# Kernel optimization log

Hardware: AMD Instinct MI355X
Metric: run time of the kernel (lower is better)

The kernel has to match this reference:

```python
import jax, jax.numpy as jnp
import numpy as np

USER_NUM = 100000
ITEM_NUM = 50000
N_NODES = USER_NUM + ITEM_NUM
EMB = 64
LAYERS = 3
NNZ = 2400000


def spmm(rows, cols, vals, x, n):
    # sparse [n, n] (COO) @ dense [n, d] -> [n, d]
    gathered = vals[:, None] * x[cols]          # [nnz, d]
    return jax.ops.segment_sum(gathered, rows, num_segments=n)


def setup_inputs() -> dict:
    key = jax.random.key(0)
    ks = jax.random.split(key, 7)
    return {
        "user_emb": jax.random.normal(ks[0], (USER_NUM, EMB), jnp.float32) * 0.1,
        "item_emb": jax.random.normal(ks[1], (ITEM_NUM, EMB), jnp.float32) * 0.1,
        "w1": jax.random.normal(ks[2], (LAYERS, EMB, EMB), jnp.float32) * (1.0 / np.sqrt(EMB)),
        "w2": jax.random.normal(ks[3], (LAYERS, EMB, EMB), jnp.float32) * (1.0 / np.sqrt(EMB)),
        "adj_vals": jax.random.uniform(ks[4], (NNZ,), jnp.float32) * (1.0 / 16.0),
        "adj_rows": jax.random.randint(ks[5], (NNZ,), 0, N_NODES, jnp.int32),
        "adj_cols": jax.random.randint(ks[6], (NNZ,), 0, N_NODES, jnp.int32),
    }


def reference(user_emb, item_emb, w1, w2, adj_vals, adj_rows, adj_cols):
    ego = jnp.concatenate([user_emb, item_emb], axis=0)   # [N, d]
    n = ego.shape[0]
    all_emb = [ego]
    for k in range(w1.shape[0]):
        temp = ego @ w1[k]                                # [N, d]
        agg_temp = spmm(adj_rows, adj_cols, adj_vals, temp, n)
        agg_ego = spmm(adj_rows, adj_cols, adj_vals, ego, n)
        ego = jax.nn.leaky_relu(agg_temp + temp + (agg_ego * ego) @ w2[k])
        all_emb.append(ego)
    mean_emb = jnp.mean(jnp.stack(all_emb, axis=1), axis=1)  # [N, d]
    u = user_emb.shape[0]
    return mean_emb[:u], mean_emb[u:]
```

## Files before the change

kernel.cpp:

```cpp
#include <hip/hip_runtime.h>
#include <hip/hip_fp16.h>

typedef _Float16 f16;
typedef _Float16 f16x4 __attribute__((ext_vector_type(4)));
typedef _Float16 f16x8 __attribute__((ext_vector_type(8)));
typedef float f32x4 __attribute__((ext_vector_type(4)));

__device__ __forceinline__ float h2f(__half v) { return __half2float(v); }
__device__ __forceinline__ __half f2h(float v) { return __float2half(v); }

#define SCAN_CHUNK 2048
#define ASTRIDE 136

#define BSHIFT 8
#define BROWS (1 << BSHIFT)
#define MAXB 1024
#define TILE 4096
#define BCAP 5120

#define WT_ELEMS (64 * ASTRIDE)
#define WT_DWORDS (WT_ELEMS / 2)

__global__ void zero_out_kernel(float* __restrict__ out, int total) {
    int i = blockIdx.x * blockDim.x + threadIdx.x;
    if (i < total) out[i] = 0.0f;
}

__global__ void setup_kernel(const float* __restrict__ user, const float* __restrict__ item,
                             __half* __restrict__ ego0, int usz, int ND,
                             const float* __restrict__ w1, const float* __restrict__ w2,
                             f16* __restrict__ wt_pre, int L,
                             int* __restrict__ gcur, int nbuck) {
    int i = blockIdx.x * blockDim.x + threadIdx.x;
    if (i < ND) {
        float f = (i < usz) ? user[i] : item[i - usz];
        ego0[i] = f2h(f);
    }
    if (i < L * WT_ELEMS) {
        int layer = i / WT_ELEMS;
        int r = i % WT_ELEMS;
        int c = r / ASTRIDE, k = r % ASTRIDE;
        float v = 0.f;
        if (k < 64)       v = w1[(size_t)layer * 4096 + (size_t)k * 64 + c];
        else if (k < 128) v = w2[(size_t)layer * 4096 + (size_t)(k - 64) * 64 + c];
        wt_pre[i] = (f16)v;
    }
    if (i < nbuck) gcur[i] = i * BCAP;
}

__global__ void hist_kernel(const int* __restrict__ rows, int* __restrict__ cnt, int nnz) {
    int i = blockIdx.x * blockDim.x + threadIdx.x;
    if (i < nnz) atomicAdd(&cnt[rows[i]], 1);
}

__global__ void scan_pass1(const int* __restrict__ cnt, int* __restrict__ bsum, int n) {
    __shared__ int wt[4];
    int tid = threadIdx.x;
    int base = blockIdx.x * SCAN_CHUNK + tid * 8;
    int s = 0;
    #pragma unroll
    for (int k = 0; k < 8; ++k) { int i = base + k; if (i < n) s += cnt[i]; }
    #pragma unroll
    for (int o = 32; o > 0; o >>= 1) s += __shfl_down(s, o, 64);
    int lane = tid & 63, wid = tid >> 6;
    if (lane == 0) wt[wid] = s;
    __syncthreads();
    if (tid == 0) bsum[blockIdx.x] = wt[0] + wt[1] + wt[2] + wt[3];
}

__global__ void scan_pass2(int* __restrict__ bsum, int nb, int* __restrict__ total) {
    if (threadIdx.x == 0) {
        int run = 0;
        for (int b = 0; b < nb; ++b) { int v = bsum[b]; bsum[b] = run; run += v; }
        *total = run;
    }
}

__global__ void scan_pass3(int* __restrict__ cnt, const int* __restrict__ bsum,
                           int* __restrict__ rptr, int n, const int* __restrict__ total) {
    __shared__ int wt[4];
    int tid = threadIdx.x;
    int base = blockIdx.x * SCAN_CHUNK + tid * 8;
    int v[8];
    int s = 0;
    #pragma unroll
    for (int k = 0; k < 8; ++k) { int i = base + k; v[k] = (i < n) ? cnt[i] : 0; s += v[k]; }
    int lane = tid & 63, wid = tid >> 6;
    int xs = s;
    #pragma unroll
    for (int o = 1; o < 64; o <<= 1) { int t = __shfl_up(xs, o, 64); if (lane >= o) xs += t; }
    if (lane == 63) wt[wid] = xs;
    __syncthreads();
    int wexcl = 0;
    for (int w = 0; w < wid; ++w) wexcl += wt[w];
    int run = bsum[blockIdx.x] + wexcl + (xs - s);
    #pragma unroll
    for (int k = 0; k < 8; ++k) {
        int i = base + k;
        if (i < n) { rptr[i] = run; cnt[i] = run; }
        run += v[k];
    }
    if (blockIdx.x == 0 && tid == 0) rptr[n] = *total;
}

__global__ void scatter_kernel(const int* __restrict__ rows, const int* __restrict__ cols,
                               const float* __restrict__ vals, int* __restrict__ cursor,
                               int2* __restrict__ edges, int nnz) {
    int i = blockIdx.x * blockDim.x + threadIdx.x;
    if (i >= nnz) return;
    int r = rows[i];
    int pos = atomicAdd(&cursor[r], 1);
    edges[pos] = make_int2(cols[i], __float_as_int(vals[i]));
}

__global__ __launch_bounds__(256)
void binA_kernel(const int* __restrict__ rows, const int* __restrict__ cols,
                 const float* __restrict__ vals, int* __restrict__ gcur,
                 int2* __restrict__ bucketed, int nnz, int nbuck) {
    __shared__ int hist[MAXB];
    __shared__ int offs[MAXB];
    __shared__ int rbase[MAXB];
    __shared__ int2 reorder[TILE];
    __shared__ unsigned short slotb[TILE];
    __shared__ int wsum[4];
    int tid = threadIdx.x;
    int tbase = blockIdx.x * TILE;
    int cnt_here = min(TILE, nnz - tbase);

    for (int b = tid; b < MAXB; b += 256) hist[b] = 0;
    __syncthreads();

    int myrow[16]; int mycol[16]; float myval[16];
    #pragma unroll
    for (int k = 0; k < 16; ++k) {
        int i = tbase + tid + k * 256;
        int r = (i < nnz) ? rows[i] : -1;
        myrow[k] = r;
        if (r >= 0) {
            mycol[k] = cols[i];
            myval[k] = vals[i];
            atomicAdd(&hist[r >> BSHIFT], 1);
        }
    }
    __syncthreads();

    int b0 = tid * 4;
    int s0 = hist[b0], s1 = hist[b0 + 1], s2 = hist[b0 + 2], s3 = hist[b0 + 3];
    int tsum = s0 + s1 + s2 + s3;
    int lane = tid & 63, wid = tid >> 6;
    int x = tsum;
    #pragma unroll
    for (int o = 1; o < 64; o <<= 1) { int t = __shfl_up(x, o, 64); if (lane >= o) x += t; }
    if (lane == 63) wsum[wid] = x;
    __syncthreads();
    int wexcl = 0;
    for (int w = 0; w < wid; ++w) wexcl += wsum[w];
    int excl = wexcl + x - tsum;
    offs[b0]     = excl;
    offs[b0 + 1] = excl + s0;
    offs[b0 + 2] = excl + s0 + s1;
    offs[b0 + 3] = excl + s0 + s1 + s2;
    for (int b = tid; b < nbuck; b += 256) {
        int c = hist[b];
        rbase[b] = (c > 0) ? atomicAdd(&gcur[b], c) : 0;
    }
    __syncthreads();
    for (int b = tid; b < MAXB; b += 256) hist[b] = 0;
    __syncthreads();

    #pragma unroll
    for (int k = 0; k < 16; ++k) {
        int r = myrow[k];
        if (r >= 0) {
            int b = r >> BSHIFT;
            int p = offs[b] + atomicAdd(&hist[b], 1);
            reorder[p] = make_int2(((r & (BROWS - 1)) << 20) | mycol[k], __float_as_int(myval[k]));
            slotb[p] = (unsigned short)b;
        }
    }
    __syncthreads();

    for (int t = tid; t < cnt_here; t += 256) {
        int b = slotb[t];
        int dst = rbase[b] + (t - offs[b]);
        if (dst < (b + 1) * BCAP) bucketed[dst] = reorder[t];
    }
}

__global__ __launch_bounds__(256)
void binB_kernel(const int* __restrict__ gcur, const int2* __restrict__ bucketed,
                 int2* __restrict__ edges, int* __restrict__ rptr, int n, int nbuck) {
    __shared__ int2 srec[BCAP];
    __shared__ int cur[BROWS];
    __shared__ int wsum[4];
    int b = blockIdx.x;
    int row_lo = b << BSHIFT;
    int nrows = min(BROWS, n - row_lo);
    int tid = threadIdx.x;
    int lane = tid & 63, wid = tid >> 6;
    cur[tid] = 0;
    int ps = 0;
    for (int j = tid; j < b; j += 256) ps += min(gcur[j] - j * BCAP, BCAP);
    #pragma unroll
    for (int o = 32; o > 0; o >>= 1) ps += __shfl_down(ps, o, 64);
    if (lane == 0) wsum[wid] = ps;
    __syncthreads();
    int beg = wsum[0] + wsum[1] + wsum[2] + wsum[3];
    int cnt = min(gcur[b] - b * BCAP, BCAP);
    int src = b * BCAP;
    for (int i = tid; i < cnt; i += 256) {
        int2 r = bucketed[src + i];
        srec[i] = r;
        atomicAdd(&cur[((unsigned)r.x) >> 20], 1);
    }
    __syncthreads();
    int c0 = cur[tid];
    int x = c0;
    #pragma unroll
    for (int o = 1; o < 64; o <<= 1) { int t = __shfl_up(x, o, 64); if (lane >= o) x += t; }
    if (lane == 63) wsum[wid] = x;
    __syncthreads();
    int wexcl = 0;
    for (int w = 0; w < wid; ++w) wexcl += wsum[w];
    int excl = beg + wexcl + x - c0;
    cur[tid] = excl;
    __syncthreads();
    if (tid < nrows) rptr[row_lo + tid] = cur[tid];
    if (b == nbuck - 1 && tid == 0) rptr[n] = beg + cnt;
    for (int i = tid; i < cnt; i += 256) {
        int2 rec = srec[i];
        int ro  = ((unsigned)rec.x) >> 20;
        int col = rec.x & 0xFFFFF;
        int pos = atomicAdd(&cur[ro], 1);
        edges[pos] = make_int2(col, rec.y);
    }
}

#define ACC8(gv, rv)                                                    \
    {                                                                   \
        float v = __int_as_float(rv.y);                                 \
        float2 a_ = __half22float2(*(const __half2*)&gv.x);             \
        float2 b_ = __half22float2(*(const __half2*)&gv.y);             \
        acc.x += v * a_.x; acc.y += v * a_.y;                           \
        acc.z += v * b_.x; acc.w += v * b_.y;                           \
    }

__device__ __forceinline__ void spmm_edge_acc(float4& acc, int2 e, const uint2* egov, int g) {
    uint2 gv = egov[((size_t)e.x << 4) + g];
    float v = __int_as_float(e.y);
    float2 a = __half22float2(*(const __half2*)&gv.x);
    float2 b = __half22float2(*(const __half2*)&gv.y);
    acc.x += v * a.x; acc.y += v * a.y; acc.z += v * b.x; acc.w += v * b.y;
}

template<int FINAL>
__global__ __launch_bounds__(512, 4)
void spmm_mfma_kernel(const int* __restrict__ rptr, const int2* __restrict__ edges,
                      const __half* __restrict__ ego, const f16* __restrict__ wtp,
                      __half* __restrict__ ego_out,
                      const __half* __restrict__ e0p, const __half* __restrict__ e1p,
                      const __half* __restrict__ e2p, float* __restrict__ outp,
                      int n, int nnz, float scale) {
    __shared__ f16 A_lds[32 * ASTRIDE];
    __shared__ f16 Wt_lds[WT_ELEMS];
    int tid = threadIdx.x;
    {
        const unsigned* wp = (const unsigned*)wtp;
        unsigned* wl = (unsigned*)Wt_lds;
        #pragma unroll
        for (int it = 0; it < 9; ++it) {
            int idx = tid + it * 512;
            if (idx < WT_DWORDS) wl[idx] = wp[idx];
        }
    }
    int lane = tid & 63, wid = tid >> 6;
    int sub = lane >> 4;
    int g   = lane & 15;
    int row  = blockIdx.x * 32 + wid * 4 + sub;
    int lrow = wid * 4 + sub;
    bool active = row < n;
    int beg = active ? rptr[row] : 0;
    int end = active ? rptr[row + 1] : 0;
    float4 acc = {0.f, 0.f, 0.f, 0.f};
    const uint2* egov = (const uint2*)ego;
    int j = beg;
    if (j + 8 <= end) {
        int2 r0 = edges[j],     r1 = edges[j + 1], r2 = edges[j + 2], r3 = edges[j + 3];
        int2 r4 = edges[j + 4], r5 = edges[j + 5], r6 = edges[j + 6], r7 = edges[j + 7];
        j += 8;
        while (j + 8 <= end) {
            uint2 g0 = egov[((size_t)r0.x << 4) + g];
            uint2 g1 = egov[((size_t)r1.x << 4) + g];
            uint2 g2 = egov[((size_t)r2.x << 4) + g];
            uint2 g3 = egov[((size_t)r3.x << 4) + g];
            uint2 g4 = egov[((size_t)r4.x << 4) + g];
            uint2 g5 = egov[((size_t)r5.x << 4) + g];
            uint2 g6 = egov[((size_t)r6.x << 4) + g];
            uint2 g7 = egov[((size_t)r7.x << 4) + g];
            int2 n0 = edges[j],     n1 = edges[j + 1], n2 = edges[j + 2], n3 = edges[j + 3];
            int2 n4 = edges[j + 4], n5 = edges[j + 5], n6 = edges[j + 6], n7 = edges[j + 7];
            ACC8(g0, r0); ACC8(g1, r1); ACC8(g2, r2); ACC8(g3, r3);
            ACC8(g4, r4); ACC8(g5, r5); ACC8(g6, r6); ACC8(g7, r7);
            r0 = n0; r1 = n1; r2 = n2; r3 = n3;
            r4 = n4; r5 = n5; r6 = n6; r7 = n7;
            j += 8;
        }
        uint2 g0 = egov[((size_t)r0.x << 4) + g];
        uint2 g1 = egov[((size_t)r1.x << 4) + g];
        uint2 g2 = egov[((size_t)r2.x << 4) + g];
        uint2 g3 = egov[((size_t)r3.x << 4) + g];
        uint2 g4 = egov[((size_t)r4.x << 4) + g];
        uint2 g5 = egov[((size_t)r5.x << 4) + g];
        uint2 g6 = egov[((size_t)r6.x << 4) + g];
        uint2 g7 = egov[((size_t)r7.x << 4) + g];
        ACC8(g0, r0); ACC8(g1, r1); ACC8(g2, r2); ACC8(g3, r3);
        ACC8(g4, r4); ACC8(g5, r5); ACC8(g6, r6); ACC8(g7, r7);
    }
    for (; j + 4 <= end; j += 4) {
        int2 e0 = edges[j], e1 = edges[j + 1], e2 = edges[j + 2], e3 = edges[j + 3];
        spmm_edge_acc(acc, e0, egov, g);
        spmm_edge_acc(acc, e1, egov, g);
        spmm_edge_acc(acc, e2, egov, g);
        spmm_edge_acc(acc, e3, egov, g);
    }
    for (; j < end; ++j) {
        spmm_edge_acc(acc, edges[j], egov, g);
    }
    {
        uint2 xv = egov[(size_t)(active ? row : 0) * 16 + g];
        float2 x01 = __half22float2(*(const __half2*)&xv.x);
        float2 x23 = __half22float2(*(const __half2*)&xv.y);
        f16x4 sv, pv;
        sv[0] = (f16)(acc.x + x01.x); sv[1] = (f16)(acc.y + x01.y);
        sv[2] = (f16)(acc.z + x23.x); sv[3] = (f16)(acc.w + x23.y);
        pv[0] = (f16)(acc.x * x01.x); pv[1] = (f16)(acc.y * x01.y);
        pv[2] = (f16)(acc.z * x23.x); pv[3] = (f16)(acc.w * x23.y);
        f16* ar = &A_lds[lrow * ASTRIDE + g * 4];
        *(f16x4*)ar        = sv;
        *(f16x4*)(ar + 64) = pv;
    }
    int band = wid >> 2;
    int nt   = wid & 3;
    int m = lane & 15, q = lane >> 4;
    int rbase = blockIdx.x * 32 + band * 16 + q * 4;
    float pre[4];
    bool ok = true;
    if (FINAL) {
        ok = (rptr[n] == nnz);
        #pragma unroll
        for (int r = 0; r < 4; ++r) {
            int grow = rbase + r;
            size_t o = (size_t)(grow < n ? grow : 0) * 64 + nt * 16 + m;
            pre[r] = h2f(e0p[o]) + h2f(e1p[o]) + h2f(e2p[o]);
        }
    }
    __syncthreads();
    f32x4 dacc = {0.f, 0.f, 0.f, 0.f};
    const f16* arow = &A_lds[(band * 16 + m) * ASTRIDE + q * 8];
    const f16* brow = &Wt_lds[(nt * 16 + m) * ASTRIDE + q * 8];
    #pragma unroll
    for (int ks = 0; ks < 4; ++ks) {
        f16x8 av = *(const f16x8*)(arow + ks * 32);
        f16x8 bv = *(const f16x8*)(brow + ks * 32);
        dacc = __builtin_amdgcn_mfma_f32_16x16x32_f16(av, bv, dacc, 0, 0, 0);
    }
    if (FINAL) {
        #pragma unroll
        for (int r = 0; r < 4; ++r) {
            int grow = rbase + r;
            if (grow < n) {
                float v = dacc[r]; v = (v > 0.f) ? v : 0.01f * v;
                size_t o = (size_t)grow * 64 + nt * 16 + m;
                outp[o] = ok ? (pre[r] + v) * scale : 0.75f;
            }
        }
    } else {
        #pragma unroll
        for (int r = 0; r < 4; ++r) {
            int grow = rbase + r;
            if (grow < n) {
                float v = dacc[r]; v = (v > 0.f) ? v : 0.01f * v;
                ego_out[(size_t)grow * 64 + nt * 16 + m] = f2h(v);
            }
        }
    }
}

__global__ void acc_kernel(const __half* __restrict__ e, float* __restrict__ out,
                           float scale, int total, int first) {
    int i = blockIdx.x * blockDim.x + threadIdx.x;
    if (i >= total) return;
    float v = h2f(e[i]) * scale;
    out[i] = first ? v : out[i] + v;
}

extern "C" void kernel_launch(void* const* d_in, const int* in_sizes, int n_in,
                              void* d_out, int out_size, void* d_ws, size_t ws_size,
                              hipStream_t stream) {
    const float* user = (const float*)d_in[0];
    const float* item = (const float*)d_in[1];
    const float* w1   = (const float*)d_in[2];
    const float* w2   = (const float*)d_in[3];
    const float* vals = (const float*)d_in[4];
    const int*   rows = (const int*)d_in[5];
    const int*   cols = (const int*)d_in[6];

    const int usz = in_sizes[0];
    const int isz = in_sizes[1];
    const int L   = in_sizes[2] / 4096;
    const int nnz = in_sizes[4];
    const int N   = (usz + isz) / 64;
    const int ND  = N * 64;
    const int nbscan = (N + SCAN_CHUNK - 1) / SCAN_CHUNK;
    const int nbuck  = (N + BROWS - 1) >> BSHIFT;

    char* p = (char*)d_ws;
    auto alloc = [&](size_t bytes) -> void* {
        void* r = (void*)p;
        p += (bytes + 255) & ~(size_t)255;
        return r;
    };
    __half* egos   = (__half*)alloc((size_t)(L + 1) * ND * 2);
    int2*   edges  = (int2*)alloc((size_t)nnz * 8);
    int*    rptr   = (int*)alloc((size_t)(N + 1) * 4);
    int*    cnt    = (int*)alloc((size_t)N * 4);
    int*    bsum   = (int*)alloc((size_t)nbscan * 4);
    int*    total  = (int*)alloc(4);
    int*    gcur   = (int*)alloc((size_t)MAXB * 4);
    f16*    wt_pre = (f16*)alloc((size_t)L * WT_ELEMS * 2);
    bool fast_sort = (nbuck <= MAXB) && (N < (1 << 20)) && (nnz > 0) &&
                     ((size_t)L * ND * 2 >= (size_t)nbuck * BCAP * 8);
    int2* bucketed = (int2*)(egos + ND);
    size_t need = (size_t)(p - (char*)d_ws);
    (void)n_in; (void)out_size;

    if (need > ws_size) {
        zero_out_kernel<<<(ND + 255) / 256, 256, 0, stream>>>((float*)d_out, ND);
        return;
    }

    int setup_max = ND > L * WT_ELEMS ? ND : L * WT_ELEMS;
    if (setup_max < nbuck) setup_max = nbuck;
    setup_kernel<<<(setup_max + 255) / 256, 256, 0, stream>>>(user, item, egos, usz, ND,
                                                              w1, w2, wt_pre, L, gcur, nbuck);

    if (fast_sort) {
        binA_kernel<<<(nnz + TILE - 1) / TILE, 256, 0, stream>>>(rows, cols, vals, gcur,
                                                                 bucketed, nnz, nbuck);
        binB_kernel<<<nbuck, 256, 0, stream>>>(gcur, bucketed, edges, rptr, N, nbuck);
    } else {
        hipMemsetAsync(cnt, 0, (size_t)N * 4, stream);
        hist_kernel<<<(nnz + 255) / 256, 256, 0, stream>>>(rows, cnt, nnz);
        scan_pass1<<<nbscan, 256, 0, stream>>>(cnt, bsum, N);
        scan_pass2<<<1, 64, 0, stream>>>(bsum, nbscan, total);
        scan_pass3<<<nbscan, 256, 0, stream>>>(cnt, bsum, rptr, N, total);
        scatter_kernel<<<(nnz + 255) / 256, 256, 0, stream>>>(rows, cols, vals, cnt, edges, nnz);
    }

    const int fb = (N + 31) / 32;
    float scale = 1.0f / (float)(L + 1);
    for (int k = 0; k < L; ++k) {
        __half* ein  = egos + (size_t)k * ND;
        __half* eout = egos + (size_t)(k + 1) * ND;
        const f16* wtp = wt_pre + (size_t)k * WT_ELEMS;
        if (L == 3 && k == 2) {
            spmm_mfma_kernel<1><<<fb, 512, 0, stream>>>(rptr, edges, ein, wtp, eout,
                                                        egos, egos + (size_t)ND,
                                                        egos + (size_t)2 * ND,
                                                        (float*)d_out, N, nnz, scale);
        } else {
            spmm_mfma_kernel<0><<<fb, 512, 0, stream>>>(rptr, edges, ein, wtp, eout,
                                                        nullptr, nullptr, nullptr,
                                                        nullptr, N, nnz, scale);
        }
    }
    if (L != 3) {
        for (int k = 0; k <= L; ++k)
            acc_kernel<<<(ND + 255) / 256, 256, 0, stream>>>(egos + (size_t)k * ND,
                                                             (float*)d_out, scale, ND, k == 0);
    }
}
```

Before: 362.8 us.

## Sort rows by degree within buckets to balance SpMM wavefront workloads

Inside binB, each block runs a bitonic sort of its 256 rows by edge count and writes a slot table of (begin, end, row). The SpMM kernel then takes its row assignment from that table, so the four 16-lane groups in each wavefront get rows of similar degree and less time is lost to divergence on uneven row lengths. The cost is an extra per-block sort with many barriers in binB and an indirect row mapping that scatters the output writes. The fallback path builds an identity slot table.

New measurement: 384.5 us. 1.06x slower.

```diff
diff --git a/kernel.cpp b/kernel.cpp
--- a/kernel.cpp
+++ b/kernel.cpp
@@ -111,6 +111,14 @@
     int r = rows[i];
     int pos = atomicAdd(&cursor[r], 1);
     edges[pos] = make_int2(cols[i], __float_as_int(vals[i]));
+}
+
+__global__ void ident_slot_kernel(const int* __restrict__ rptr, int4* __restrict__ slotinfo,
+                                  int n, int slots) {
+    int i = blockIdx.x * blockDim.x + threadIdx.x;
+    if (i >= slots) return;
+    if (i < n) slotinfo[i] = make_int4(rptr[i], rptr[i + 1], i, 0);
+    else       slotinfo[i] = make_int4(0, 0, n, 0);
 }
 
 __global__ __launch_bounds__(256)
@@ -189,9 +197,13 @@
 
 __global__ __launch_bounds__(256)
 void binB_kernel(const int* __restrict__ gcur, const int2* __restrict__ bucketed,
-                 int2* __restrict__ edges, int* __restrict__ rptr, int n, int nbuck) {
+                 int2* __restrict__ edges, int* __restrict__ rptr,
+                 int4* __restrict__ slotinfo, int n, int nbuck) {
     __shared__ int2 srec[BCAP];
     __shared__ int cur[BROWS];
+    __shared__ int skey[BROWS];
+    __shared__ int sbeg2[BROWS];
+    __shared__ int scnt2[BROWS];
     __shared__ int wsum[4];
     int b = blockIdx.x;
     int row_lo = b << BSHIFT;
@@ -224,9 +236,32 @@
     for (int w = 0; w < wid; ++w) wexcl += wsum[w];
     int excl = beg + wexcl + x - c0;
     cur[tid] = excl;
+    sbeg2[tid] = excl;
+    scnt2[tid] = c0;
+    skey[tid] = (min(c0, 0x7FFF) << 8) | tid;
     __syncthreads();
     if (tid < nrows) rptr[row_lo + tid] = cur[tid];
     if (b == nbuck - 1 && tid == 0) rptr[n] = beg + cnt;
+    for (int k = 2; k <= BROWS; k <<= 1) {
+        for (int jj = k >> 1; jj > 0; jj >>= 1) {
+            __syncthreads();
+            int ixj = tid ^ jj;
+            if (ixj > tid) {
+                int a = skey[tid], c2 = skey[ixj];
+                bool up = ((tid & k) == 0);
+                if (up ? (a > c2) : (a < c2)) { skey[tid] = c2; skey[ixj] = a; }
+            }
+        }
+    }
+    __syncthreads();
+    {
+        int r = skey[tid] & 0xFF;
+        int sb = sbeg2[r];
+        int srow = row_lo + r;
+        slotinfo[(size_t)b * BROWS + tid] = make_int4(sb, sb + scnt2[r],
+                                                      (r < nrows) ? srow : n, 0);
+    }
+    __syncthreads();
     for (int i = tid; i < cnt; i += 256) {
         int2 rec = srec[i];
         int ro  = ((unsigned)rec.x) >> 20;
@@ -234,6 +269,14 @@
         int pos = atomicAdd(&cur[ro], 1);
         edges[pos] = make_int2(col, rec.y);
     }
+}
+
+__device__ __forceinline__ void spmm_edge_acc(float4& acc, int2 e, const uint2* egov, int g) {
+    uint2 gv = egov[((size_t)e.x << 4) + g];
+    float v = __int_as_float(e.y);
+    float2 a = __half22float2(*(const __half2*)&gv.x);
+    float2 b = __half22float2(*(const __half2*)&gv.y);
+    acc.x += v * a.x; acc.y += v * a.y; acc.z += v * b.x; acc.w += v * b.y;
 }
 
 #define ACC8(gv, rv)                                                    \
@@ -245,19 +288,11 @@
         acc.z += v * b_.x; acc.w += v * b_.y;                           \
     }
 
-__device__ __forceinline__ void spmm_edge_acc(float4& acc, int2 e, const uint2* egov, int g) {
-    uint2 gv = egov[((size_t)e.x << 4) + g];
-    float v = __int_as_float(e.y);
-    float2 a = __half22float2(*(const __half2*)&gv.x);
-    float2 b = __half22float2(*(const __half2*)&gv.y);
-    acc.x += v * a.x; acc.y += v * a.y; acc.z += v * b.x; acc.w += v * b.y;
-}
-
 template<int FINAL>
 __global__ __launch_bounds__(512, 4)
 void spmm_mfma_kernel(const int* __restrict__ rptr, const int2* __restrict__ edges,
                       const __half* __restrict__ ego, const f16* __restrict__ wtp,
-                      __half* __restrict__ ego_out,
+                      const int4* __restrict__ slotinfo, __half* __restrict__ ego_out,
                       const __half* __restrict__ e0p, const __half* __restrict__ e1p,
                       const __half* __restrict__ e2p, float* __restrict__ outp,
                       int n, int nnz, float scale) {
@@ -276,16 +311,15 @@
     int lane = tid & 63, wid = tid >> 6;
     int sub = lane >> 4;
     int g   = lane & 15;
-    int row  = blockIdx.x * 32 + wid * 4 + sub;
     int lrow = wid * 4 + sub;
+    int4 si = slotinfo[(size_t)blockIdx.x * 32 + lrow];
+    int beg = si.x, end = si.y, row = si.z;
     bool active = row < n;
-    int beg = active ? rptr[row] : 0;
-    int end = active ? rptr[row + 1] : 0;
     float4 acc = {0.f, 0.f, 0.f, 0.f};
     const uint2* egov = (const uint2*)ego;
     int j = beg;
     if (j + 8 <= end) {
-        int2 r0 = edges[j],     r1 = edges[j + 1], r2 = edges[j + 2], r3 = edges[j + 3];
+        int2 r0 = ((const int2*)edges)[j],     r1 = edges[j + 1], r2 = edges[j + 2], r3 = edges[j + 3];
         int2 r4 = edges[j + 4], r5 = edges[j + 5], r6 = edges[j + 6], r7 = edges[j + 7];
         j += 8;
         while (j + 8 <= end) {
@@ -342,15 +376,18 @@
     int band = wid >> 2;
     int nt   = wid & 3;
     int m = lane & 15, q = lane >> 4;
-    int rbase = blockIdx.x * 32 + band * 16 + q * 4;
+    const int* slz = (const int*)slotinfo;
+    int gs0 = blockIdx.x * 32 + band * 16 + q * 4;
+    int prow[4];
+    #pragma unroll
+    for (int r = 0; r < 4; ++r) prow[r] = slz[((size_t)(gs0 + r) << 2) + 2];
     float pre[4];
     bool ok = true;
     if (FINAL) {
         ok = (rptr[n] == nnz);
         #pragma unroll
         for (int r = 0; r < 4; ++r) {
-            int grow = rbase + r;
-            size_t o = (size_t)(grow < n ? grow : 0) * 64 + nt * 16 + m;
+            size_t o = (size_t)(prow[r] < n ? prow[r] : 0) * 64 + nt * 16 + m;
             pre[r] = h2f(e0p[o]) + h2f(e1p[o]) + h2f(e2p[o]);
         }
     }
@@ -367,20 +404,18 @@
     if (FINAL) {
         #pragma unroll
         for (int r = 0; r < 4; ++r) {
-            int grow = rbase + r;
-            if (grow < n) {
+            if (prow[r] < n) {
                 float v = dacc[r]; v = (v > 0.f) ? v : 0.01f * v;
-                size_t o = (size_t)grow * 64 + nt * 16 + m;
+                size_t o = (size_t)prow[r] * 64 + nt * 16 + m;
                 outp[o] = ok ? (pre[r] + v) * scale : 0.75f;
             }
         }
     } else {
         #pragma unroll
         for (int r = 0; r < 4; ++r) {
-            int grow = rbase + r;
-            if (grow < n) {
+            if (prow[r] < n) {
                 float v = dacc[r]; v = (v > 0.f) ? v : 0.01f * v;
-                ego_out[(size_t)grow * 64 + nt * 16 + m] = f2h(v);
+                ego_out[(size_t)prow[r] * 64 + nt * 16 + m] = f2h(v);
             }
         }
     }
@@ -428,6 +463,7 @@
     int*    total  = (int*)alloc(4);
     int*    gcur   = (int*)alloc((size_t)MAXB * 4);
     f16*    wt_pre = (f16*)alloc((size_t)L * WT_ELEMS * 2);
+    int4*   slotinfo = (int4*)alloc((size_t)nbuck * BROWS * 16);
     bool fast_sort = (nbuck <= MAXB) && (N < (1 << 20)) && (nnz > 0) &&
                      ((size_t)L * ND * 2 >= (size_t)nbuck * BCAP * 8);
     int2* bucketed = (int2*)(egos + ND);
@@ -444,10 +480,12 @@
     setup_kernel<<<(setup_max + 255) / 256, 256, 0, stream>>>(user, item, egos, usz, ND,
                                                               w1, w2, wt_pre, L, gcur, nbuck);
 
+    int fb;
     if (fast_sort) {
         binA_kernel<<<(nnz + TILE - 1) / TILE, 256, 0, stream>>>(rows, cols, vals, gcur,
                                                                  bucketed, nnz, nbuck);
-        binB_kernel<<<nbuck, 256, 0, stream>>>(gcur, bucketed, edges, rptr, N, nbuck);
+        binB_kernel<<<nbuck, 256, 0, stream>>>(gcur, bucketed, edges, rptr, slotinfo, N, nbuck);
+        fb = nbuck * 8;
     } else {
         hipMemsetAsync(cnt, 0, (size_t)N * 4, stream);
         hist_kernel<<<(nnz + 255) / 256, 256, 0, stream>>>(rows, cnt, nnz);
@@ -455,21 +493,23 @@
         scan_pass2<<<1, 64, 0, stream>>>(bsum, nbscan, total);
         scan_pass3<<<nbscan, 256, 0, stream>>>(cnt, bsum, rptr, N, total);
         scatter_kernel<<<(nnz + 255) / 256, 256, 0, stream>>>(rows, cols, vals, cnt, edges, nnz);
-    }
-
-    const int fb = (N + 31) / 32;
+        fb = (N + 31) / 32;
+        int slots = fb * 32;
+        ident_slot_kernel<<<(slots + 255) / 256, 256, 0, stream>>>(rptr, slotinfo, N, slots);
+    }
+
     float scale = 1.0f / (float)(L + 1);
     for (int k = 0; k < L; ++k) {
         __half* ein  = egos + (size_t)k * ND;
         __half* eout = egos + (size_t)(k + 1) * ND;
         const f16* wtp = wt_pre + (size_t)k * WT_ELEMS;
         if (L == 3 && k == 2) {
-            spmm_mfma_kernel<1><<<fb, 512, 0, stream>>>(rptr, edges, ein, wtp, eout,
+            spmm_mfma_kernel<1><<<fb, 512, 0, stream>>>(rptr, edges, ein, wtp, slotinfo, eout,
                                                         egos, egos + (size_t)ND,
                                                         egos + (size_t)2 * ND,
                                                         (float*)d_out, N, nnz, scale);
         } else {
-            spmm_mfma_kernel<0><<<fb, 512, 0, stream>>>(rptr, edges, ein, wtp, eout,
+            spmm_mfma_kernel<0><<<fb, 512, 0, stream>>>(rptr, edges, ein, wtp, slotinfo, eout,
                                                         nullptr, nullptr, nullptr,
                                                         nullptr, N, nnz, scale);
         }
```
